# Optimization experiments

Measured on AMD Instinct MI355X. Metric: run time of the kernel, lower is better.

## Reference

```python
import jax, jax.numpy as jnp
import numpy as np

N_NODES = 50000
N_EDGES = 800000
IN_DIM = 128
HID = 256
OUT_DIM = 64
N_CONV = 4  # n_hidden_layers - 1
BN_EPS = 1e-5


def setup_inputs() -> dict:
    key = jax.random.key(0)
    ks = jax.random.split(key, 16)
    h = jax.random.normal(ks[0], (N_NODES, IN_DIM), dtype=jnp.float32)
    src = jax.random.randint(ks[1], (N_EDGES,), 0, N_NODES, dtype=jnp.int32)
    dst = jax.random.randint(ks[2], (N_EDGES,), 0, N_NODES, dtype=jnp.int32)
    s_in = 1.0 / np.sqrt(IN_DIM)
    s_h = 1.0 / np.sqrt(HID)
    conv0_W1 = jax.random.normal(ks[3], (IN_DIM, HID), jnp.float32) * s_in
    convs_W1 = jax.random.normal(ks[4], (N_CONV - 1, HID, HID), jnp.float32) * s_h
    convs_W2 = jax.random.normal(ks[5], (N_CONV, HID, HID), jnp.float32) * s_h
    bn1_gamma = jnp.ones((N_CONV, HID), jnp.float32)
    bn1_beta = jnp.zeros((N_CONV, HID), jnp.float32)
    bn2_gamma = jnp.ones((N_CONV, HID), jnp.float32)
    bn2_beta = jnp.zeros((N_CONV, HID), jnp.float32)
    pred0_W = jax.random.normal(ks[6], (IN_DIM, OUT_DIM), jnp.float32) * s_in
    pred0_b = jnp.zeros((OUT_DIM,), jnp.float32)
    preds_W = jax.random.normal(ks[7], (N_CONV, HID, OUT_DIM), jnp.float32) * s_h
    preds_b = jnp.zeros((N_CONV, OUT_DIM), jnp.float32)
    return {
        "h": h, "conv0_W1": conv0_W1, "convs_W1": convs_W1, "convs_W2": convs_W2,
        "bn1_gamma": bn1_gamma, "bn1_beta": bn1_beta,
        "bn2_gamma": bn2_gamma, "bn2_beta": bn2_beta,
        "pred0_W": pred0_W, "pred0_b": pred0_b,
        "preds_W": preds_W, "preds_b": preds_b,
        "src": src, "dst": dst,
    }


def _bn(x, gamma, beta):
    # training-mode batchnorm over the node axis (biased variance, like torch)
    m = jnp.mean(x, axis=0)
    v = jnp.var(x, axis=0)
    return (x - m) * jax.lax.rsqrt(v + BN_EPS) * gamma + beta


def reference(h, conv0_W1, convs_W1, convs_W2, bn1_gamma, bn1_beta,
              bn2_gamma, bn2_beta, pred0_W, pred0_b, preds_W, preds_b,
              src, dst):
    n = h.shape[0]
    hidden_rep = [h]
    x = h
    for i in range(N_CONV):
        # GINConv (eps=0): x_v + sum over incoming edges of x_src
        agg = x + jax.ops.segment_sum(x[src], dst, num_segments=n)
        W1 = conv0_W1 if i == 0 else convs_W1[i - 1]
        z = jax.nn.relu(_bn(agg @ W1, bn1_gamma[i], bn1_beta[i])) @ convs_W2[i]
        x = jax.nn.relu(_bn(z, bn2_gamma[i], bn2_beta[i]))
        hidden_rep.append(x)
    # jumping-knowledge linear heads (dropout is identity in eval mode)
    out = hidden_rep[0] @ pred0_W + pred0_b
    for i in range(N_CONV):
        out = out + hidden_rep[i + 1] @ preds_W[i] + preds_b[i]
    return out
```

## Files before the change

### kernel.cpp

```cpp
#include <hip/hip_runtime.h>

#define N_NODES 50000
#define MPAD    50176
#define N_EDGES 800000
#define IN_DIM 128
#define HID 256
#define OUT_DIM 64
#define N_CONV 4
#define KCAT 1152

typedef __bf16 bf16;
typedef __attribute__((ext_vector_type(8))) __bf16 bf16x8;
typedef __attribute__((ext_vector_type(4))) float f32x4;
typedef unsigned short ushort_t;

__device__ __forceinline__ unsigned short f2b(float f){
  unsigned u = __float_as_uint(f);
  u += 0x7fffu + ((u >> 16) & 1u);
  return (unsigned short)(u >> 16);
}
__device__ __forceinline__ float b2f_lo(unsigned v){ return __uint_as_float(v << 16); }
__device__ __forceinline__ float b2f_hi(unsigned v){ return __uint_as_float(v & 0xffff0000u); }

__device__ __forceinline__ void stage16(const void* g, void* l){
  __builtin_amdgcn_global_load_lds((const __attribute__((address_space(1))) unsigned int*)g,
                                   (__attribute__((address_space(3))) unsigned int*)l, 16, 0, 0);
}

__global__ void k_count(const int* __restrict__ dst, int* __restrict__ cnt, int ne){
  int e = blockIdx.x*blockDim.x + threadIdx.x;
  if (e < ne) atomicAdd(&cnt[dst[e]], 1);
}

__global__ void k_scan1(const int* __restrict__ cnt, int* __restrict__ scanned,
                        int* __restrict__ bsum, int n){
  int i = blockIdx.x*256 + threadIdx.x;
  int v = (i < n) ? cnt[i] : 0;
  int lane = threadIdx.x & 63;
  #pragma unroll
  for (int off = 1; off < 64; off <<= 1){
    int t = __shfl_up(v, off, 64);
    if (lane >= off) v += t;
  }
  __shared__ int wsum[4];
  int wv = threadIdx.x >> 6;
  if (lane == 63) wsum[wv] = v;
  __syncthreads();
  if (threadIdx.x == 0){
    int s = 0;
    #pragma unroll
    for (int k = 0; k < 4; ++k){ int t = wsum[k]; wsum[k] = s; s += t; }
    bsum[blockIdx.x] = s;
  }
  __syncthreads();
  v += wsum[wv];
  if (i < n) scanned[i] = v;
}

__global__ void k_scan2(int* __restrict__ bsum, int nb){
  __shared__ int sd[256];
  int i = threadIdx.x;
  sd[i] = (i < nb) ? bsum[i] : 0;
  __syncthreads();
  #pragma unroll
  for (int off = 1; off < 256; off <<= 1){
    int t = (i >= off) ? sd[i-off] : 0;
    __syncthreads();
    sd[i] += t;
    __syncthreads();
  }
  if (i < nb) bsum[i] = sd[i];
}

__global__ void k_scan3(const int* __restrict__ scanned, const int* __restrict__ bsum,
                        const int* __restrict__ cnt, int* __restrict__ row_ptr,
                        int* __restrict__ cursor, int n){
  int i = blockIdx.x*256 + threadIdx.x;
  if (i < n){
    int off = (blockIdx.x > 0) ? bsum[blockIdx.x-1] : 0;
    int inc = scanned[i] + off;
    row_ptr[i+1] = inc;
    cursor[i] = inc - cnt[i];
  }
  if (i == 0) row_ptr[0] = 0;
}

__global__ void k_fill(const int* __restrict__ src, const int* __restrict__ dst,
                       int* __restrict__ cursor, int* __restrict__ esrc, int ne){
  int e = blockIdx.x*blockDim.x + threadIdx.x;
  if (e < ne){
    int p = atomicAdd(&cursor[dst[e]], 1);
    esrc[p] = src[e];
  }
}

template<int D>
__global__ void k_agg(const ushort_t* __restrict__ x, const int* __restrict__ rp,
                      const int* __restrict__ es, ushort_t* __restrict__ agg, int n){
  int gw = (int)((blockIdx.x*(size_t)blockDim.x + threadIdx.x) >> 6);
  int lane = threadIdx.x & 63;
  if (gw >= n) return;
  if (D == 256){
    const uint2* xp = (const uint2*)x; const int S = KCAT/4;
    uint2 v = xp[(size_t)gw*S + lane];
    float a0=b2f_lo(v.x), a1=b2f_hi(v.x), a2=b2f_lo(v.y), a3=b2f_hi(v.y);
    float c0=0.f, c1=0.f, c2=0.f, c3=0.f;
    int e = rp[gw], e1 = rp[gw+1];
    for (; e + 8 <= e1; e += 8){
      uint2 w[8];
      #pragma unroll
      for (int u = 0; u < 8; ++u) w[u] = xp[(size_t)es[e+u]*S + lane];
      #pragma unroll
      for (int u = 0; u < 8; u += 2){
        a0 += b2f_lo(w[u].x);   a1 += b2f_hi(w[u].x);   a2 += b2f_lo(w[u].y);   a3 += b2f_hi(w[u].y);
        c0 += b2f_lo(w[u+1].x); c1 += b2f_hi(w[u+1].x); c2 += b2f_lo(w[u+1].y); c3 += b2f_hi(w[u+1].y);
      }
    }
    for (; e + 2 <= e1; e += 2){
      uint2 w0 = xp[(size_t)es[e]*S + lane];
      uint2 w1 = xp[(size_t)es[e+1]*S + lane];
      a0 += b2f_lo(w0.x); a1 += b2f_hi(w0.x); a2 += b2f_lo(w0.y); a3 += b2f_hi(w0.y);
      c0 += b2f_lo(w1.x); c1 += b2f_hi(w1.x); c2 += b2f_lo(w1.y); c3 += b2f_hi(w1.y);
    }
    if (e < e1){
      uint2 w0 = xp[(size_t)es[e]*S + lane];
      a0 += b2f_lo(w0.x); a1 += b2f_hi(w0.x); a2 += b2f_lo(w0.y); a3 += b2f_hi(w0.y);
    }
    a0 += c0; a1 += c1; a2 += c2; a3 += c3;
    unsigned o0 = (unsigned)f2b(a0) | ((unsigned)f2b(a1) << 16);
    unsigned o1 = (unsigned)f2b(a2) | ((unsigned)f2b(a3) << 16);
    *(uint2*)(agg + (size_t)gw*256 + lane*4) = make_uint2(o0, o1);
  } else {
    const unsigned* xp = (const unsigned*)x; const int S = KCAT/2;
    unsigned v = xp[(size_t)gw*S + lane];
    float a0 = b2f_lo(v), a1 = b2f_hi(v);
    float c0 = 0.f, c1 = 0.f;
    int e = rp[gw], e1 = rp[gw+1];
    for (; e + 8 <= e1; e += 8){
      unsigned w[8];
      #pragma unroll
      for (int u = 0; u < 8; ++u) w[u] = xp[(size_t)es[e+u]*S + lane];
      #pragma unroll
      for (int u = 0; u < 8; u += 2){
        a0 += b2f_lo(w[u]);   a1 += b2f_hi(w[u]);
        c0 += b2f_lo(w[u+1]); c1 += b2f_hi(w[u+1]);
      }
    }
    for (; e + 2 <= e1; e += 2){
      unsigned w0 = xp[(size_t)es[e]*S + lane];
      unsigned w1 = xp[(size_t)es[e+1]*S + lane];
      a0 += b2f_lo(w0); a1 += b2f_hi(w0);
      c0 += b2f_lo(w1); c1 += b2f_hi(w1);
    }
    if (e < e1){
      unsigned w0 = xp[(size_t)es[e]*S + lane];
      a0 += b2f_lo(w0); a1 += b2f_hi(w0);
    }
    a0 += c0; a1 += c1;
    unsigned o = (unsigned)f2b(a0) | ((unsigned)f2b(a1) << 16);
    *(unsigned*)(agg + (size_t)gw*128 + lane*2) = o;
  }
}

__global__ void k_bnrelu(const ushort_t* __restrict__ t, const float* __restrict__ sums,
                         const float* __restrict__ g, const float* __restrict__ b,
                         ushort_t* __restrict__ o, int ostride, int M, float invM){
  int idx = blockIdx.x*blockDim.x + threadIdx.x;
  if (idx >= M*(HID/8)) return;
  int row = idx >> 5, cg = (idx & 31) * 8;
  uint4 v = *(const uint4*)(t + (size_t)row*HID + cg);
  unsigned wv[4] = {v.x, v.y, v.z, v.w};
  unsigned ov[4];
  #pragma unroll
  for (int p = 0; p < 4; ++p){
    int c0 = cg + 2*p, c1 = c0 + 1;
    float m0 = sums[c0]*invM, m1 = sums[c1]*invM;
    float r0 = rsqrtf(sums[HID+c0]*invM - m0*m0 + 1e-5f);
    float r1 = rsqrtf(sums[HID+c1]*invM - m1*m1 + 1e-5f);
    float y0 = (b2f_lo(wv[p]) - m0)*r0*g[c0] + b[c0];
    float y1 = (b2f_hi(wv[p]) - m1)*r1*g[c1] + b[c1];
    y0 = y0 > 0.f ? y0 : 0.f; y1 = y1 > 0.f ? y1 : 0.f;
    ov[p] = (unsigned)f2b(y0) | ((unsigned)f2b(y1) << 16);
  }
  *(uint4*)(o + (size_t)row*ostride + cg) = make_uint4(ov[0], ov[1], ov[2], ov[3]);
}

__global__ void k_f2b(const float* __restrict__ in, ushort_t* __restrict__ xcat, int n8){
  int idx = blockIdx.x*blockDim.x + threadIdx.x;
  if (idx >= n8) return;
  int row = idx >> 4, cg = (idx & 15) * 8;
  float4 a = *(const float4*)(in + (size_t)row*IN_DIM + cg);
  float4 c = *(const float4*)(in + (size_t)row*IN_DIM + cg + 4);
  unsigned o0 = (unsigned)f2b(a.x) | ((unsigned)f2b(a.y) << 16);
  unsigned o1 = (unsigned)f2b(a.z) | ((unsigned)f2b(a.w) << 16);
  unsigned o2 = (unsigned)f2b(c.x) | ((unsigned)f2b(c.y) << 16);
  unsigned o3 = (unsigned)f2b(c.z) | ((unsigned)f2b(c.w) << 16);
  *(uint4*)(xcat + (size_t)row*KCAT + cg) = make_uint4(o0, o1, o2, o3);
}

__global__ void k_wprep(const float* __restrict__ c0W1, const float* __restrict__ cW1,
                        const float* __restrict__ cW2, const float* __restrict__ p0W,
                        const float* __restrict__ pW,
                        const float* __restrict__ p0b, const float* __restrict__ pb,
                        ushort_t* __restrict__ wb, ushort_t* __restrict__ whead,
                        float* __restrict__ ball){
  int m = blockIdx.y;
  if (m == 13){
    if (blockIdx.x == 0 && threadIdx.x < OUT_DIM){
      int c = threadIdx.x;
      float v = p0b[c];
      #pragma unroll
      for (int i = 0; i < N_CONV; ++i) v += pb[i*OUT_DIM + c];
      ball[c] = v;
    }
    return;
  }
  const float* src; int R, C; ushort_t* dst; int dstride, dcol;
  if (m == 0){       src = c0W1;              R = 128; C = 256; dst = wb;                       dstride = 128;  dcol = 0; }
  else if (m <= 3){  src = cW1 + (m-1)*65536; R = 256; C = 256; dst = wb + 32768 + (m-1)*65536; dstride = 256;  dcol = 0; }
  else if (m <= 7){  src = cW2 + (m-4)*65536; R = 256; C = 256; dst = wb + 229376 + (m-4)*65536;dstride = 256;  dcol = 0; }
  else if (m == 8){  src = p0W;               R = 128; C = 64;  dst = whead;                    dstride = KCAT; dcol = 0; }
  else {             src = pW + (m-9)*16384;  R = 256; C = 64;  dst = whead;                    dstride = KCAT; dcol = 128 + (m-9)*256; }
  int tx = R/64, tiles = tx * (C/64);
  int t = blockIdx.x;
  if (t >= tiles) return;
  int sr0 = (t % tx)*64, sc0 = (t / tx)*64;
  __shared__ float ld[64][65];
  int c = threadIdx.x & 63, rq = threadIdx.x >> 6;
  #pragma unroll
  for (int i = 0; i < 16; ++i){
    int rr = i*4 + rq;
    ld[rr][c] = src[(size_t)(sr0+rr)*C + sc0 + c];
  }
  __syncthreads();
  #pragma unroll
  for (int i = 0; i < 16; ++i){
    int rr = i*4 + rq;
    dst[(size_t)(sc0+rr)*dstride + dcol + sr0 + c] = f2b(ld[c][rr]);
  }
}

template<int BM, int BN, int MODE>
__global__ __launch_bounds__((BM/64)*(BN/64)*64)
void k_mgemm(const bf16* __restrict__ A, const bf16* __restrict__ BT,
             void* __restrict__ Cv, const float* __restrict__ bias,
             float* __restrict__ sums, const float* __restrict__ asums,
             const float* __restrict__ ag, const float* __restrict__ ab,
             int M, int N, int K, float invM)
{
  constexpr int NW  = (BM/64)*(BN/64);
  constexpr int WNT = BN/64;
  constexpr int ACH = BM/16, BCH = BN/16;
  __shared__ __align__(16) bf16 As[2*BM*32];
  __shared__ __align__(16) bf16 Bs[2*BN*32];
  __shared__ float sAf[MODE==2?256:1];
  __shared__ float tAf[MODE==2?256:1];
  const int tid = threadIdx.x;
  const int wid = tid >> 6, l = tid & 63;
  const int wm = wid / WNT, wn = wid % WNT;
  const int m0 = blockIdx.y * BM, n0 = blockIdx.x * BN;
  const int r = l & 15, q = l >> 4;
  const int fragByte = ((q ^ ((r >> 1) & 3)) << 4);
  const int wrow = l >> 2;
  const int wk = (((l & 3) ^ ((l >> 3) & 3)) << 3);

  if constexpr (MODE == 2){
    if (tid < 256){
      float m = asums[tid] * invM;
      float var = asums[256 + tid] * invM - m*m;
      float s = rsqrtf(var + 1e-5f) * ag[tid];
      sAf[tid] = s;
      tAf[tid] = ab[tid] - m*s;
    }
    __syncthreads();
  }

  auto STAGE = [&](int buf, int k0){
    #pragma unroll
    for (int c = 0; c < ACH/NW; ++c){
      int ch = wid + c*NW;
      if constexpr (MODE == 2){
        int grow = m0 + ch*16 + wrow;
        uint4 raw = *(const uint4*)(A + (size_t)grow*K + (k0 + wk));
        int kc = k0 + wk;
        unsigned rv[4] = {raw.x, raw.y, raw.z, raw.w};
        unsigned ov[4];
        #pragma unroll
        for (int p = 0; p < 4; ++p){
          int c0 = kc + 2*p, c1 = c0 + 1;
          float y0 = fmaf(b2f_lo(rv[p]), sAf[c0], tAf[c0]);
          float y1 = fmaf(b2f_hi(rv[p]), sAf[c1], tAf[c1]);
          y0 = y0 > 0.f ? y0 : 0.f; y1 = y1 > 0.f ? y1 : 0.f;
          ov[p] = (unsigned)f2b(y0) | ((unsigned)f2b(y1) << 16);
        }
        if (grow >= M){ ov[0]=0; ov[1]=0; ov[2]=0; ov[3]=0; }
        *(uint4*)((char*)As + buf*(BM*64) + ch*1024 + l*16) = make_uint4(ov[0],ov[1],ov[2],ov[3]);
      } else {
        const bf16* g = A + (size_t)(m0 + ch*16 + wrow)*K + (k0 + wk);
        stage16(g, (char*)As + buf*(BM*64) + ch*1024);
      }
    }
    #pragma unroll
    for (int c = 0; c < BCH/NW; ++c){
      int ch = wid + c*NW;
      const bf16* g = BT + (size_t)(n0 + ch*16 + wrow)*K + (k0 + wk);
      stage16(g, (char*)Bs + buf*(BN*64) + ch*1024);
    }
  };

  f32x4 acc[4][4] = {};
  const int nt = K >> 5;
  STAGE(0, 0);
  for (int t = 0; t < nt; ++t){
    int cur = t & 1;
    __syncthreads();
    if (t + 1 < nt) STAGE(cur ^ 1, (t + 1) << 5);
    bf16x8 af[4], bfr[4];
    #pragma unroll
    for (int mf = 0; mf < 4; ++mf)
      af[mf] = *(const bf16x8*)((const char*)As + cur*(BM*64) + (wm*64 + mf*16 + r)*64 + fragByte);
    #pragma unroll
    for (int nf = 0; nf < 4; ++nf)
      bfr[nf] = *(const bf16x8*)((const char*)Bs + cur*(BN*64) + (wn*64 + nf*16 + r)*64 + fragByte);
    #pragma unroll
    for (int mf = 0; mf < 4; ++mf)
      #pragma unroll
      for (int nf = 0; nf < 4; ++nf)
        acc[mf][nf] = __builtin_amdgcn_mfma_f32_16x16x32_bf16(af[mf], bfr[nf], acc[mf][nf], 0, 0, 0);
  }

  if (MODE == 0 || MODE == 2){
    ushort_t* Cb = (ushort_t*)Cv;
    float s1[4] = {0.f,0.f,0.f,0.f}, s2[4] = {0.f,0.f,0.f,0.f};
    #pragma unroll
    for (int mf = 0; mf < 4; ++mf){
      #pragma unroll
      for (int j = 0; j < 4; ++j){
        int row = m0 + wm*64 + mf*16 + q*4 + j;
        #pragma unroll
        for (int nf = 0; nf < 4; ++nf){
          unsigned short us = f2b(acc[mf][nf][j]);
          float vr = __uint_as_float((unsigned)us << 16);
          s1[nf] += vr; s2[nf] = fmaf(vr, vr, s2[nf]);
          Cb[(size_t)row*N + n0 + wn*64 + nf*16 + r] = us;
        }
      }
    }
    #pragma unroll
    for (int nf = 0; nf < 4; ++nf){
      float a = s1[nf], c = s2[nf];
      a += __shfl_xor(a, 16, 64); a += __shfl_xor(a, 32, 64);
      c += __shfl_xor(c, 16, 64); c += __shfl_xor(c, 32, 64);
      if (q == 0){
        int col = n0 + wn*64 + nf*16 + r;
        atomicAdd(&sums[col], a);
        atomicAdd(&sums[256 + col], c);
      }
    }
  } else {
    float* C = (float*)Cv;
    #pragma unroll
    for (int mf = 0; mf < 4; ++mf){
      #pragma unroll
      for (int j = 0; j < 4; ++j){
        int row = m0 + wm*64 + mf*16 + q*4 + j;
        if (row >= M) continue;
        #pragma unroll
        for (int nf = 0; nf < 4; ++nf){
          int col = n0 + wn*64 + nf*16 + r;
          C[(size_t)row*N + col] = acc[mf][nf][j] + bias[col];
        }
      }
    }
  }
}

extern "C" void kernel_launch(void* const* d_in, const int* in_sizes, int n_in,
                              void* d_out, int out_size, void* d_ws, size_t ws_size,
                              hipStream_t stream){
  const float* h    = (const float*)d_in[0];
  const float* c0W1 = (const float*)d_in[1];
  const float* cW1  = (const float*)d_in[2];
  const float* cW2  = (const float*)d_in[3];
  const float* bn1g = (const float*)d_in[4];
  const float* bn1b = (const float*)d_in[5];
  const float* bn2g = (const float*)d_in[6];
  const float* bn2b = (const float*)d_in[7];
  const float* p0W  = (const float*)d_in[8];
  const float* p0b  = (const float*)d_in[9];
  const float* pW   = (const float*)d_in[10];
  const float* pb   = (const float*)d_in[11];
  const int* src    = (const int*)d_in[12];
  const int* dst    = (const int*)d_in[13];
  float* out = (float*)d_out;

  char* w = (char*)d_ws;
  auto alloc = [&](size_t bytes)->char*{ char* p = w; w += (bytes + 255) & ~(size_t)255; return p; };
  ushort_t* xcat = (ushort_t*)alloc((size_t)MPAD*KCAT*2);
  ushort_t* aggb = (ushort_t*)alloc((size_t)MPAD*HID*2);
  ushort_t* tt   = (ushort_t*)alloc((size_t)MPAD*HID*2);
  ushort_t* wb   = (ushort_t*)alloc((size_t)491520*2);
  ushort_t* whead= (ushort_t*)alloc((size_t)OUT_DIM*KCAT*2);
  int* row_ptr   = (int*)alloc((N_NODES+1)*4);
  int* cursor    = (int*)alloc(N_NODES*4);
  int* counts    = (int*)alloc(N_NODES*4);
  int* esrc      = (int*)alloc(N_EDGES*4);
  int* scanned   = (int*)alloc(N_NODES*4);
  int* bsum      = (int*)alloc(256*4);
  float* sums8   = (float*)alloc(8*512*4);
  float* ball    = (float*)alloc(OUT_DIM*4);

  hipMemsetAsync(aggb + (size_t)N_NODES*IN_DIM, 0, (size_t)(MPAD-N_NODES)*IN_DIM*2, stream);
  hipMemsetAsync(aggb + (size_t)N_NODES*HID,    0, (size_t)(MPAD-N_NODES)*HID*2,    stream);
  hipMemsetAsync(sums8, 0, 8*512*4, stream);

  const int NB = (N_NODES + 255) / 256;
  hipMemsetAsync(counts, 0, N_NODES*4, stream);
  k_count<<<(N_EDGES+255)/256, 256, 0, stream>>>(dst, counts, N_EDGES);
  k_scan1<<<NB, 256, 0, stream>>>(counts, scanned, bsum, N_NODES);
  k_scan2<<<1, 256, 0, stream>>>(bsum, NB);
  k_scan3<<<NB, 256, 0, stream>>>(scanned, bsum, counts, row_ptr, cursor, N_NODES);
  k_fill<<<(N_EDGES+255)/256, 256, 0, stream>>>(src, dst, cursor, esrc, N_EDGES);

  k_wprep<<<dim3(16, 14), 256, 0, stream>>>(c0W1, cW1, cW2, p0W, pW, p0b, pb, wb, whead, ball);
  k_f2b<<<(N_NODES*16 + 255)/256, 256, 0, stream>>>(h, xcat, N_NODES*16);

  const float invM = 1.0f / (float)N_NODES;
  for (int i = 0; i < N_CONV; ++i){
    int K1 = (i == 0) ? IN_DIM : HID;
    const ushort_t* xin = (i == 0) ? xcat : (xcat + 128 + (size_t)(i-1)*HID);
    if (i == 0)
      k_agg<IN_DIM><<<(N_NODES*64+255)/256, 256, 0, stream>>>(xin, row_ptr, esrc, aggb, N_NODES);
    else
      k_agg<HID><<<(N_NODES*64+255)/256, 256, 0, stream>>>(xin, row_ptr, esrc, aggb, N_NODES);

    float* sums1 = sums8 + (size_t)(2*i)*512;
    float* sums2 = sums8 + (size_t)(2*i+1)*512;

    const ushort_t* W1T = (i == 0) ? wb : (wb + 32768 + (size_t)(i-1)*65536);
    k_mgemm<64, 256, 0><<<dim3(1, MPAD/64), 256, 0, stream>>>(
        (const bf16*)aggb, (const bf16*)W1T, tt, nullptr, sums1,
        nullptr, nullptr, nullptr, N_NODES, HID, K1, invM);

    const ushort_t* W2T = wb + 229376 + (size_t)i*65536;
    k_mgemm<64, 256, 2><<<dim3(1, MPAD/64), 256, 0, stream>>>(
        (const bf16*)tt, (const bf16*)W2T, aggb, nullptr, sums2,
        sums1, bn1g + i*HID, bn1b + i*HID, N_NODES, HID, HID, invM);

    k_bnrelu<<<(N_NODES*32 + 255)/256, 256, 0, stream>>>(
        aggb, sums2, bn2g + i*HID, bn2b + i*HID, xcat + 128 + (size_t)i*HID, KCAT, N_NODES, invM);
  }

  k_mgemm<128, 64, 1><<<dim3(1, MPAD/128), 128, 0, stream>>>(
      (const bf16*)xcat, (const bf16*)whead, out, ball, nullptr,
      nullptr, nullptr, nullptr, N_NODES, OUT_DIM, KCAT, invM);
}
```

Baseline: 675.5 us.

## Load GEMM B fragments directly from global into registers; merge memsets into one kernel

The GEMM no longer stages the B (weight) tile through shared memory. Each wave reads its B MFMA fragments straight from global memory into registers, double-buffered across k-steps, which cuts LDS traffic and LDS footprint and may raise occupancy. The cost is uncoalesced 16-byte global loads of B that each wave repeats, and more registers held. Separately, three hipMemsetAsync calls are replaced by one fused zeroing kernel to reduce launch overhead.

```diff
diff --git a/kernel.cpp b/kernel.cpp
--- a/kernel.cpp
+++ b/kernel.cpp
@@ -92,6 +92,15 @@
     int p = atomicAdd(&cursor[dst[e]], 1);
     esrc[p] = src[e];
   }
+}
+
+__global__ void k_zero(char* p0, int n0, char* p1, int n1, char* p2, int n2){
+  int i = (blockIdx.x*blockDim.x + threadIdx.x) * 16;
+  if (i < n0) *(uint4*)(p0 + i) = make_uint4(0,0,0,0);
+  i -= n0;
+  if (i >= 0 && i < n1) *(uint4*)(p1 + i) = make_uint4(0,0,0,0);
+  i -= n1;
+  if (i >= 0 && i < n2) *(uint4*)(p2 + i) = make_uint4(0,0,0,0);
 }
 
 template<int D>
@@ -250,9 +259,8 @@
 {
   constexpr int NW  = (BM/64)*(BN/64);
   constexpr int WNT = BN/64;
-  constexpr int ACH = BM/16, BCH = BN/16;
+  constexpr int ACH = BM/16;
   __shared__ __align__(16) bf16 As[2*BM*32];
-  __shared__ __align__(16) bf16 Bs[2*BN*32];
   __shared__ float sAf[MODE==2?256:1];
   __shared__ float tAf[MODE==2?256:1];
   const int tid = threadIdx.x;
@@ -275,7 +283,7 @@
     __syncthreads();
   }
 
-  auto STAGE = [&](int buf, int k0){
+  auto STAGE_A = [&](int buf, int k0){
     #pragma unroll
     for (int c = 0; c < ACH/NW; ++c){
       int ch = wid + c*NW;
@@ -300,33 +308,38 @@
         stage16(g, (char*)As + buf*(BM*64) + ch*1024);
       }
     }
-    #pragma unroll
-    for (int c = 0; c < BCH/NW; ++c){
-      int ch = wid + c*NW;
-      const bf16* g = BT + (size_t)(n0 + ch*16 + wrow)*K + (k0 + wk);
-      stage16(g, (char*)Bs + buf*(BN*64) + ch*1024);
-    }
+  };
+
+  const bf16* Bbase = BT + (size_t)(n0 + wn*64 + r)*K + q*8;
+  auto LOADB = [&](bf16x8* d, int k0){
+    #pragma unroll
+    for (int nf = 0; nf < 4; ++nf)
+      d[nf] = *(const bf16x8*)(Bbase + (size_t)nf*16*K + k0);
   };
 
   f32x4 acc[4][4] = {};
   const int nt = K >> 5;
-  STAGE(0, 0);
+  bf16x8 bcur[4], bnxt[4];
+  STAGE_A(0, 0);
+  LOADB(bcur, 0);
   for (int t = 0; t < nt; ++t){
     int cur = t & 1;
     __syncthreads();
-    if (t + 1 < nt) STAGE(cur ^ 1, (t + 1) << 5);
-    bf16x8 af[4], bfr[4];
+    if (t + 1 < nt){
+      STAGE_A(cur ^ 1, (t + 1) << 5);
+      LOADB(bnxt, (t + 1) << 5);
+    }
+    bf16x8 af[4];
     #pragma unroll
     for (int mf = 0; mf < 4; ++mf)
       af[mf] = *(const bf16x8*)((const char*)As + cur*(BM*64) + (wm*64 + mf*16 + r)*64 + fragByte);
     #pragma unroll
-    for (int nf = 0; nf < 4; ++nf)
-      bfr[nf] = *(const bf16x8*)((const char*)Bs + cur*(BN*64) + (wn*64 + nf*16 + r)*64 + fragByte);
-    #pragma unroll
     for (int mf = 0; mf < 4; ++mf)
       #pragma unroll
       for (int nf = 0; nf < 4; ++nf)
-        acc[mf][nf] = __builtin_amdgcn_mfma_f32_16x16x32_bf16(af[mf], bfr[nf], acc[mf][nf], 0, 0, 0);
+        acc[mf][nf] = __builtin_amdgcn_mfma_f32_16x16x32_bf16(af[mf], bcur[nf], acc[mf][nf], 0, 0, 0);
+    #pragma unroll
+    for (int nf = 0; nf < 4; ++nf) bcur[nf] = bnxt[nf];
   }
 
   if (MODE == 0 || MODE == 2){
@@ -410,9 +423,15 @@
   float* sums8   = (float*)alloc(8*512*4);
   float* ball    = (float*)alloc(OUT_DIM*4);
 
-  hipMemsetAsync(aggb + (size_t)N_NODES*IN_DIM, 0, (size_t)(MPAD-N_NODES)*IN_DIM*2, stream);
-  hipMemsetAsync(aggb + (size_t)N_NODES*HID,    0, (size_t)(MPAD-N_NODES)*HID*2,    stream);
-  hipMemsetAsync(sums8, 0, 8*512*4, stream);
+  {
+    const int PADR = MPAD - N_NODES;
+    int n0 = PADR*IN_DIM*2, n1 = PADR*HID*2, n2 = 8*512*4;
+    int chunks = (n0 + n1 + n2) / 16;
+    k_zero<<<(chunks + 255)/256, 256, 0, stream>>>(
+        (char*)(aggb + (size_t)N_NODES*IN_DIM), n0,
+        (char*)(aggb + (size_t)N_NODES*HID), n1,
+        (char*)sums8, n2);
+  }
 
   const int NB = (N_NODES + 255) / 256;
   hipMemsetAsync(counts, 0, N_NODES*4, stream);
```

Result: slower. 710.0 us (+5.1%).

## Fuse BN2+ReLU of previous layer into next layer's neighbor aggregation

Applied to the files above, without the earlier changes.

The separate BN2+ReLU pass for layers 0-2 is removed. The next layer's aggregation kernel now reads the raw pre-BN GEMM output, applies the scale/shift and ReLU on the fly for the self row and every gathered neighbor, and also writes the normalized self row into the concatenated feature buffer. To make this work, the aggregation output and the GEMM1 output alternate between two buffers across layers, and only the last layer keeps a standalone BN+ReLU pass. The separate memsets are also folded into one zeroing kernel. This saves a full read/write of the activations per layer, at the cost of recomputing the normalization once per edge gather.

```diff
diff --git a/kernel.cpp b/kernel.cpp
--- a/kernel.cpp
+++ b/kernel.cpp
@@ -94,72 +94,108 @@
   }
 }
 
-template<int D>
-__global__ void k_agg(const ushort_t* __restrict__ x, const int* __restrict__ rp,
-                      const int* __restrict__ es, ushort_t* __restrict__ agg, int n){
+__global__ void k_zero(char* p0, int n0, char* p1, int n1, char* p2, int n2, char* p3, int n3){
+  int i = (blockIdx.x*blockDim.x + threadIdx.x) * 16;
+  if (i < n0) *(uint4*)(p0 + i) = make_uint4(0,0,0,0);
+  i -= n0;
+  if (i >= 0 && i < n1) *(uint4*)(p1 + i) = make_uint4(0,0,0,0);
+  i -= n1;
+  if (i >= 0 && i < n2) *(uint4*)(p2 + i) = make_uint4(0,0,0,0);
+  i -= n2;
+  if (i >= 0 && i < n3) *(uint4*)(p3 + i) = make_uint4(0,0,0,0);
+}
+
+__global__ void k_agg0(const ushort_t* __restrict__ x, const int* __restrict__ rp,
+                       const int* __restrict__ es, ushort_t* __restrict__ agg, int n){
   int gw = (int)((blockIdx.x*(size_t)blockDim.x + threadIdx.x) >> 6);
   int lane = threadIdx.x & 63;
   if (gw >= n) return;
-  if (D == 256){
-    const uint2* xp = (const uint2*)x; const int S = KCAT/4;
-    uint2 v = xp[(size_t)gw*S + lane];
-    float a0=b2f_lo(v.x), a1=b2f_hi(v.x), a2=b2f_lo(v.y), a3=b2f_hi(v.y);
-    float c0=0.f, c1=0.f, c2=0.f, c3=0.f;
-    int e = rp[gw], e1 = rp[gw+1];
-    for (; e + 8 <= e1; e += 8){
-      uint2 w[8];
-      #pragma unroll
-      for (int u = 0; u < 8; ++u) w[u] = xp[(size_t)es[e+u]*S + lane];
-      #pragma unroll
-      for (int u = 0; u < 8; u += 2){
-        a0 += b2f_lo(w[u].x);   a1 += b2f_hi(w[u].x);   a2 += b2f_lo(w[u].y);   a3 += b2f_hi(w[u].y);
-        c0 += b2f_lo(w[u+1].x); c1 += b2f_hi(w[u+1].x); c2 += b2f_lo(w[u+1].y); c3 += b2f_hi(w[u+1].y);
-      }
-    }
-    for (; e + 2 <= e1; e += 2){
-      uint2 w0 = xp[(size_t)es[e]*S + lane];
-      uint2 w1 = xp[(size_t)es[e+1]*S + lane];
-      a0 += b2f_lo(w0.x); a1 += b2f_hi(w0.x); a2 += b2f_lo(w0.y); a3 += b2f_hi(w0.y);
-      c0 += b2f_lo(w1.x); c1 += b2f_hi(w1.x); c2 += b2f_lo(w1.y); c3 += b2f_hi(w1.y);
-    }
-    if (e < e1){
-      uint2 w0 = xp[(size_t)es[e]*S + lane];
-      a0 += b2f_lo(w0.x); a1 += b2f_hi(w0.x); a2 += b2f_lo(w0.y); a3 += b2f_hi(w0.y);
-    }
-    a0 += c0; a1 += c1; a2 += c2; a3 += c3;
-    unsigned o0 = (unsigned)f2b(a0) | ((unsigned)f2b(a1) << 16);
-    unsigned o1 = (unsigned)f2b(a2) | ((unsigned)f2b(a3) << 16);
-    *(uint2*)(agg + (size_t)gw*256 + lane*4) = make_uint2(o0, o1);
-  } else {
-    const unsigned* xp = (const unsigned*)x; const int S = KCAT/2;
-    unsigned v = xp[(size_t)gw*S + lane];
-    float a0 = b2f_lo(v), a1 = b2f_hi(v);
-    float c0 = 0.f, c1 = 0.f;
-    int e = rp[gw], e1 = rp[gw+1];
-    for (; e + 8 <= e1; e += 8){
-      unsigned w[8];
-      #pragma unroll
-      for (int u = 0; u < 8; ++u) w[u] = xp[(size_t)es[e+u]*S + lane];
-      #pragma unroll
-      for (int u = 0; u < 8; u += 2){
-        a0 += b2f_lo(w[u]);   a1 += b2f_hi(w[u]);
-        c0 += b2f_lo(w[u+1]); c1 += b2f_hi(w[u+1]);
-      }
-    }
-    for (; e + 2 <= e1; e += 2){
-      unsigned w0 = xp[(size_t)es[e]*S + lane];
-      unsigned w1 = xp[(size_t)es[e+1]*S + lane];
-      a0 += b2f_lo(w0); a1 += b2f_hi(w0);
-      c0 += b2f_lo(w1); c1 += b2f_hi(w1);
-    }
-    if (e < e1){
-      unsigned w0 = xp[(size_t)es[e]*S + lane];
-      a0 += b2f_lo(w0); a1 += b2f_hi(w0);
-    }
-    a0 += c0; a1 += c1;
-    unsigned o = (unsigned)f2b(a0) | ((unsigned)f2b(a1) << 16);
-    *(unsigned*)(agg + (size_t)gw*128 + lane*2) = o;
-  }
+  const unsigned* xp = (const unsigned*)x; const int S = KCAT/2;
+  unsigned v = xp[(size_t)gw*S + lane];
+  float a0 = b2f_lo(v), a1 = b2f_hi(v);
+  float c0 = 0.f, c1 = 0.f;
+  int e = rp[gw], e1 = rp[gw+1];
+  for (; e + 8 <= e1; e += 8){
+    unsigned w[8];
+    #pragma unroll
+    for (int u = 0; u < 8; ++u) w[u] = xp[(size_t)es[e+u]*S + lane];
+    #pragma unroll
+    for (int u = 0; u < 8; u += 2){
+      a0 += b2f_lo(w[u]);   a1 += b2f_hi(w[u]);
+      c0 += b2f_lo(w[u+1]); c1 += b2f_hi(w[u+1]);
+    }
+  }
+  for (; e + 2 <= e1; e += 2){
+    unsigned w0 = xp[(size_t)es[e]*S + lane];
+    unsigned w1 = xp[(size_t)es[e+1]*S + lane];
+    a0 += b2f_lo(w0); a1 += b2f_hi(w0);
+    c0 += b2f_lo(w1); c1 += b2f_hi(w1);
+  }
+  if (e < e1){
+    unsigned w0 = xp[(size_t)es[e]*S + lane];
+    a0 += b2f_lo(w0); a1 += b2f_hi(w0);
+  }
+  a0 += c0; a1 += c1;
+  unsigned o = (unsigned)f2b(a0) | ((unsigned)f2b(a1) << 16);
+  *(unsigned*)(agg + (size_t)gw*128 + lane*2) = o;
+}
+
+__global__ void k_aggbn(const ushort_t* __restrict__ x, const int* __restrict__ rp,
+                        const int* __restrict__ es, ushort_t* __restrict__ agg,
+                        ushort_t* __restrict__ xc,
+                        const float* __restrict__ sums, const float* __restrict__ g,
+                        const float* __restrict__ b, float invM, int n){
+  int gw = (int)((blockIdx.x*(size_t)blockDim.x + threadIdx.x) >> 6);
+  int lane = threadIdx.x & 63;
+  if (gw >= n) return;
+  float sc[4], sh[4];
+  #pragma unroll
+  for (int j = 0; j < 4; ++j){
+    int c = lane*4 + j;
+    float m = sums[c]*invM;
+    float var = sums[256 + c]*invM - m*m;
+    float r = rsqrtf(var + 1e-5f);
+    sc[j] = r * g[c];
+    sh[j] = b[c] - m*sc[j];
+  }
+  const uint2* xp = (const uint2*)x;
+  uint2 v = xp[(size_t)gw*64 + lane];
+  float a0 = fmaxf(fmaf(b2f_lo(v.x), sc[0], sh[0]), 0.f);
+  float a1 = fmaxf(fmaf(b2f_hi(v.x), sc[1], sh[1]), 0.f);
+  float a2 = fmaxf(fmaf(b2f_lo(v.y), sc[2], sh[2]), 0.f);
+  float a3 = fmaxf(fmaf(b2f_hi(v.y), sc[3], sh[3]), 0.f);
+  unsigned so0 = (unsigned)f2b(a0) | ((unsigned)f2b(a1) << 16);
+  unsigned so1 = (unsigned)f2b(a2) | ((unsigned)f2b(a3) << 16);
+  *(uint2*)(xc + (size_t)gw*KCAT + lane*4) = make_uint2(so0, so1);
+  float c0 = 0.f, c1 = 0.f, c2 = 0.f, c3 = 0.f;
+  int e = rp[gw], e1 = rp[gw+1];
+  for (; e + 8 <= e1; e += 8){
+    uint2 w[8];
+    #pragma unroll
+    for (int u = 0; u < 8; ++u) w[u] = xp[(size_t)es[e+u]*64 + lane];
+    #pragma unroll
+    for (int u = 0; u < 8; u += 2){
+      a0 += fmaxf(fmaf(b2f_lo(w[u].x),   sc[0], sh[0]), 0.f);
+      a1 += fmaxf(fmaf(b2f_hi(w[u].x),   sc[1], sh[1]), 0.f);
+      a2 += fmaxf(fmaf(b2f_lo(w[u].y),   sc[2], sh[2]), 0.f);
+      a3 += fmaxf(fmaf(b2f_hi(w[u].y),   sc[3], sh[3]), 0.f);
+      c0 += fmaxf(fmaf(b2f_lo(w[u+1].x), sc[0], sh[0]), 0.f);
+      c1 += fmaxf(fmaf(b2f_hi(w[u+1].x), sc[1], sh[1]), 0.f);
+      c2 += fmaxf(fmaf(b2f_lo(w[u+1].y), sc[2], sh[2]), 0.f);
+      c3 += fmaxf(fmaf(b2f_hi(w[u+1].y), sc[3], sh[3]), 0.f);
+    }
+  }
+  for (; e < e1; ++e){
+    uint2 w0 = xp[(size_t)es[e]*64 + lane];
+    a0 += fmaxf(fmaf(b2f_lo(w0.x), sc[0], sh[0]), 0.f);
+    a1 += fmaxf(fmaf(b2f_hi(w0.x), sc[1], sh[1]), 0.f);
+    a2 += fmaxf(fmaf(b2f_lo(w0.y), sc[2], sh[2]), 0.f);
+    a3 += fmaxf(fmaf(b2f_hi(w0.y), sc[3], sh[3]), 0.f);
+  }
+  a0 += c0; a1 += c1; a2 += c2; a3 += c3;
+  unsigned o0 = (unsigned)f2b(a0) | ((unsigned)f2b(a1) << 16);
+  unsigned o1 = (unsigned)f2b(a2) | ((unsigned)f2b(a3) << 16);
+  *(uint2*)(agg + (size_t)gw*256 + lane*4) = make_uint2(o0, o1);
 }
 
 __global__ void k_bnrelu(const ushort_t* __restrict__ t, const float* __restrict__ sums,
@@ -410,12 +446,17 @@
   float* sums8   = (float*)alloc(8*512*4);
   float* ball    = (float*)alloc(OUT_DIM*4);
 
-  hipMemsetAsync(aggb + (size_t)N_NODES*IN_DIM, 0, (size_t)(MPAD-N_NODES)*IN_DIM*2, stream);
-  hipMemsetAsync(aggb + (size_t)N_NODES*HID,    0, (size_t)(MPAD-N_NODES)*HID*2,    stream);
-  hipMemsetAsync(sums8, 0, 8*512*4, stream);
+  {
+    const int PADR = MPAD - N_NODES;
+    int n0 = PADR*IN_DIM*2, n1 = PADR*HID*2, n2 = 8*512*4, n3 = N_NODES*4;
+    int chunks = (n0 + n1 + n2 + n3) / 16;
+    k_zero<<<(chunks + 255)/256, 256, 0, stream>>>(
+        (char*)(aggb + (size_t)N_NODES*IN_DIM), n0,
+        (char*)(aggb + (size_t)N_NODES*HID), n1,
+        (char*)sums8, n2, (char*)counts, n3);
+  }
 
   const int NB = (N_NODES + 255) / 256;
-  hipMemsetAsync(counts, 0, N_NODES*4, stream);
   k_count<<<(N_EDGES+255)/256, 256, 0, stream>>>(dst, counts, N_EDGES);
   k_scan1<<<NB, 256, 0, stream>>>(counts, scanned, bsum, N_NODES);
   k_scan2<<<1, 256, 0, stream>>>(bsum, NB);
@@ -426,30 +467,37 @@
   k_f2b<<<(N_NODES*16 + 255)/256, 256, 0, stream>>>(h, xcat, N_NODES*16);
 
   const float invM = 1.0f / (float)N_NODES;
+  ushort_t* raw = nullptr;
   for (int i = 0; i < N_CONV; ++i){
     int K1 = (i == 0) ? IN_DIM : HID;
-    const ushort_t* xin = (i == 0) ? xcat : (xcat + 128 + (size_t)(i-1)*HID);
-    if (i == 0)
-      k_agg<IN_DIM><<<(N_NODES*64+255)/256, 256, 0, stream>>>(xin, row_ptr, esrc, aggb, N_NODES);
-    else
-      k_agg<HID><<<(N_NODES*64+255)/256, 256, 0, stream>>>(xin, row_ptr, esrc, aggb, N_NODES);
-
+    ushort_t* aout = (i == 0) ? aggb : ((i & 1) ? tt : aggb);
+    ushort_t* g1o  = (i & 1) ? aggb : tt;
     float* sums1 = sums8 + (size_t)(2*i)*512;
     float* sums2 = sums8 + (size_t)(2*i+1)*512;
 
+    if (i == 0)
+      k_agg0<<<(N_NODES*64+255)/256, 256, 0, stream>>>(xcat, row_ptr, esrc, aggb, N_NODES);
+    else
+      k_aggbn<<<(N_NODES*64+255)/256, 256, 0, stream>>>(
+          raw, row_ptr, esrc, aout, xcat + 128 + (size_t)(i-1)*HID,
+          sums8 + (size_t)(2*(i-1)+1)*512, bn2g + (i-1)*HID, bn2b + (i-1)*HID,
+          invM, N_NODES);
+
     const ushort_t* W1T = (i == 0) ? wb : (wb + 32768 + (size_t)(i-1)*65536);
     k_mgemm<64, 256, 0><<<dim3(1, MPAD/64), 256, 0, stream>>>(
-        (const bf16*)aggb, (const bf16*)W1T, tt, nullptr, sums1,
+        (const bf16*)aout, (const bf16*)W1T, g1o, nullptr, sums1,
         nullptr, nullptr, nullptr, N_NODES, HID, K1, invM);
 
     const ushort_t* W2T = wb + 229376 + (size_t)i*65536;
     k_mgemm<64, 256, 2><<<dim3(1, MPAD/64), 256, 0, stream>>>(
-        (const bf16*)tt, (const bf16*)W2T, aggb, nullptr, sums2,
+        (const bf16*)g1o, (const bf16*)W2T, aout, nullptr, sums2,
         sums1, bn1g + i*HID, bn1b + i*HID, N_NODES, HID, HID, invM);
-
-    k_bnrelu<<<(N_NODES*32 + 255)/256, 256, 0, stream>>>(
-        aggb, sums2, bn2g + i*HID, bn2b + i*HID, xcat + 128 + (size_t)i*HID, KCAT, N_NODES, invM);
-  }
+    raw = aout;
+  }
+
+  k_bnrelu<<<(N_NODES*32 + 255)/256, 256, 0, stream>>>(
+      raw, sums8 + 7*512, bn2g + 3*HID, bn2b + 3*HID,
+      xcat + 128 + (size_t)3*HID, KCAT, N_NODES, invM);
 
   k_mgemm<128, 64, 1><<<dim3(1, MPAD/128), 128, 0, stream>>>(
       (const bf16*)xcat, (const bf16*)whead, out, ball, nullptr,
```

After: 686.2 us. About the same (+1.6%).

## Fuse final BN+ReLU into head GEMM and merge memsets into one zero kernel

Applied to the files above, without the earlier changes.

The last layer's BN2+ReLU pass is skipped. The head GEMM gains a mode that reads the last K-slice directly from the pre-BN buffer and applies the BN scale/shift and ReLU while staging it into shared memory. This removes one elementwise kernel launch plus its write and re-read of a 50k x 256 bf16 slice. The four separate memsets are also merged into a single zeroing kernel to cut launch overhead. In exchange, the head GEMM does extra ALU work on the last K tiles and takes a branch in its staging loop.

```diff
diff --git a/kernel.cpp b/kernel.cpp
--- a/kernel.cpp
+++ b/kernel.cpp
@@ -92,6 +92,17 @@
     int p = atomicAdd(&cursor[dst[e]], 1);
     esrc[p] = src[e];
   }
+}
+
+__global__ void k_zero(char* p0, int n0, char* p1, int n1, char* p2, int n2, char* p3, int n3){
+  int i = (blockIdx.x*blockDim.x + threadIdx.x) * 16;
+  if (i < n0) *(uint4*)(p0 + i) = make_uint4(0,0,0,0);
+  i -= n0;
+  if (i >= 0 && i < n1) *(uint4*)(p1 + i) = make_uint4(0,0,0,0);
+  i -= n1;
+  if (i >= 0 && i < n2) *(uint4*)(p2 + i) = make_uint4(0,0,0,0);
+  i -= n2;
+  if (i >= 0 && i < n3) *(uint4*)(p3 + i) = make_uint4(0,0,0,0);
 }
 
 template<int D>
@@ -246,6 +257,7 @@
              void* __restrict__ Cv, const float* __restrict__ bias,
              float* __restrict__ sums, const float* __restrict__ asums,
              const float* __restrict__ ag, const float* __restrict__ ab,
+             const bf16* __restrict__ A2,
              int M, int N, int K, float invM)
 {
   constexpr int NW  = (BM/64)*(BN/64);
@@ -253,8 +265,8 @@
   constexpr int ACH = BM/16, BCH = BN/16;
   __shared__ __align__(16) bf16 As[2*BM*32];
   __shared__ __align__(16) bf16 Bs[2*BN*32];
-  __shared__ float sAf[MODE==2?256:1];
-  __shared__ float tAf[MODE==2?256:1];
+  __shared__ float sAf[(MODE>=2)?256:1];
+  __shared__ float tAf[(MODE>=2)?256:1];
   const int tid = threadIdx.x;
   const int wid = tid >> 6, l = tid & 63;
   const int wm = wid / WNT, wn = wid % WNT;
@@ -264,39 +276,51 @@
   const int wrow = l >> 2;
   const int wk = (((l & 3) ^ ((l >> 3) & 3)) << 3);
 
-  if constexpr (MODE == 2){
-    if (tid < 256){
-      float m = asums[tid] * invM;
-      float var = asums[256 + tid] * invM - m*m;
-      float s = rsqrtf(var + 1e-5f) * ag[tid];
-      sAf[tid] = s;
-      tAf[tid] = ab[tid] - m*s;
+  if constexpr (MODE >= 2){
+    for (int c = tid; c < 256; c += NW*64){
+      float m = asums[c] * invM;
+      float var = asums[256 + c] * invM - m*m;
+      float s = rsqrtf(var + 1e-5f) * ag[c];
+      sAf[c] = s;
+      tAf[c] = ab[c] - m*s;
     }
     __syncthreads();
   }
+
+  auto REGSTAGE_A = [&](int buf, int ch, const bf16* srcRow, int kc){
+    uint4 raw = *(const uint4*)(srcRow);
+    unsigned rv[4] = {raw.x, raw.y, raw.z, raw.w};
+    unsigned ov[4];
+    #pragma unroll
+    for (int p = 0; p < 4; ++p){
+      int c0 = kc + 2*p, c1 = c0 + 1;
+      float y0 = fmaf(b2f_lo(rv[p]), sAf[c0], tAf[c0]);
+      float y1 = fmaf(b2f_hi(rv[p]), sAf[c1], tAf[c1]);
+      y0 = y0 > 0.f ? y0 : 0.f; y1 = y1 > 0.f ? y1 : 0.f;
+      ov[p] = (unsigned)f2b(y0) | ((unsigned)f2b(y1) << 16);
+    }
+    int grow = m0 + ch*16 + wrow;
+    if (grow >= M){ ov[0]=0; ov[1]=0; ov[2]=0; ov[3]=0; }
+    *(uint4*)((char*)As + buf*(BM*64) + ch*1024 + l*16) = make_uint4(ov[0],ov[1],ov[2],ov[3]);
+  };
 
   auto STAGE = [&](int buf, int k0){
     #pragma unroll
     for (int c = 0; c < ACH/NW; ++c){
       int ch = wid + c*NW;
+      int grow = m0 + ch*16 + wrow;
       if constexpr (MODE == 2){
-        int grow = m0 + ch*16 + wrow;
-        uint4 raw = *(const uint4*)(A + (size_t)grow*K + (k0 + wk));
-        int kc = k0 + wk;
-        unsigned rv[4] = {raw.x, raw.y, raw.z, raw.w};
-        unsigned ov[4];
-        #pragma unroll
-        for (int p = 0; p < 4; ++p){
-          int c0 = kc + 2*p, c1 = c0 + 1;
-          float y0 = fmaf(b2f_lo(rv[p]), sAf[c0], tAf[c0]);
-          float y1 = fmaf(b2f_hi(rv[p]), sAf[c1], tAf[c1]);
-          y0 = y0 > 0.f ? y0 : 0.f; y1 = y1 > 0.f ? y1 : 0.f;
-          ov[p] = (unsigned)f2b(y0) | ((unsigned)f2b(y1) << 16);
+        REGSTAGE_A(buf, ch, A + (size_t)grow*K + (k0 + wk), k0 + wk);
+      } else if constexpr (MODE == 3){
+        if (k0 < 896){
+          const bf16* g = A + (size_t)grow*K + (k0 + wk);
+          stage16(g, (char*)As + buf*(BM*64) + ch*1024);
+        } else {
+          int kc = k0 - 896 + wk;
+          REGSTAGE_A(buf, ch, A2 + (size_t)grow*HID + kc, kc);
         }
-        if (grow >= M){ ov[0]=0; ov[1]=0; ov[2]=0; ov[3]=0; }
-        *(uint4*)((char*)As + buf*(BM*64) + ch*1024 + l*16) = make_uint4(ov[0],ov[1],ov[2],ov[3]);
       } else {
-        const bf16* g = A + (size_t)(m0 + ch*16 + wrow)*K + (k0 + wk);
+        const bf16* g = A + (size_t)grow*K + (k0 + wk);
         stage16(g, (char*)As + buf*(BM*64) + ch*1024);
       }
     }
@@ -410,12 +434,17 @@
   float* sums8   = (float*)alloc(8*512*4);
   float* ball    = (float*)alloc(OUT_DIM*4);
 
-  hipMemsetAsync(aggb + (size_t)N_NODES*IN_DIM, 0, (size_t)(MPAD-N_NODES)*IN_DIM*2, stream);
-  hipMemsetAsync(aggb + (size_t)N_NODES*HID,    0, (size_t)(MPAD-N_NODES)*HID*2,    stream);
-  hipMemsetAsync(sums8, 0, 8*512*4, stream);
+  {
+    const int PADR = MPAD - N_NODES;
+    int n0 = PADR*IN_DIM*2, n1 = PADR*HID*2, n2 = 8*512*4, n3 = N_NODES*4;
+    int chunks = (n0 + n1 + n2 + n3) / 16;
+    k_zero<<<(chunks + 255)/256, 256, 0, stream>>>(
+        (char*)(aggb + (size_t)N_NODES*IN_DIM), n0,
+        (char*)(aggb + (size_t)N_NODES*HID), n1,
+        (char*)sums8, n2, (char*)counts, n3);
+  }
 
   const int NB = (N_NODES + 255) / 256;
-  hipMemsetAsync(counts, 0, N_NODES*4, stream);
   k_count<<<(N_EDGES+255)/256, 256, 0, stream>>>(dst, counts, N_EDGES);
   k_scan1<<<NB, 256, 0, stream>>>(counts, scanned, bsum, N_NODES);
   k_scan2<<<1, 256, 0, stream>>>(bsum, NB);
@@ -440,18 +469,20 @@
     const ushort_t* W1T = (i == 0) ? wb : (wb + 32768 + (size_t)(i-1)*65536);
     k_mgemm<64, 256, 0><<<dim3(1, MPAD/64), 256, 0, stream>>>(
         (const bf16*)aggb, (const bf16*)W1T, tt, nullptr, sums1,
-        nullptr, nullptr, nullptr, N_NODES, HID, K1, invM);
+        nullptr, nullptr, nullptr, nullptr, N_NODES, HID, K1, invM);
 
     const ushort_t* W2T = wb + 229376 + (size_t)i*65536;
     k_mgemm<64, 256, 2><<<dim3(1, MPAD/64), 256, 0, stream>>>(
         (const bf16*)tt, (const bf16*)W2T, aggb, nullptr, sums2,
-        sums1, bn1g + i*HID, bn1b + i*HID, N_NODES, HID, HID, invM);
-
-    k_bnrelu<<<(N_NODES*32 + 255)/256, 256, 0, stream>>>(
-        aggb, sums2, bn2g + i*HID, bn2b + i*HID, xcat + 128 + (size_t)i*HID, KCAT, N_NODES, invM);
-  }
-
-  k_mgemm<128, 64, 1><<<dim3(1, MPAD/128), 128, 0, stream>>>(
+        sums1, bn1g + i*HID, bn1b + i*HID, nullptr, N_NODES, HID, HID, invM);
+
+    if (i < 3)
+      k_bnrelu<<<(N_NODES*32 + 255)/256, 256, 0, stream>>>(
+          aggb, sums2, bn2g + i*HID, bn2b + i*HID, xcat + 128 + (size_t)i*HID, KCAT, N_NODES, invM);
+  }
+
+  k_mgemm<128, 64, 3><<<dim3(1, MPAD/128), 128, 0, stream>>>(
       (const bf16*)xcat, (const bf16*)whead, out, ball, nullptr,
-      nullptr, nullptr, nullptr, N_NODES, OUT_DIM, KCAT, invM);
-}
+      sums8 + 7*512, bn2g + 3*HID, bn2b + 3*HID, (const bf16*)aggb,
+      N_NODES, OUT_DIM, KCAT, invM);
+}
```

Result: no change. 677.0 us (+0.2%).
